# Kernel optimization log

Measured on AMD Instinct MI355X. Metric: run time of the kernel, lower is better.

Reference implementation:

```python
import jax, jax.numpy as jnp
import numpy as np
from jax import lax

B, T, A, L, H, FD = 32, 64, 6, 32, 128, 256


def setup_inputs() -> dict:
    key = jax.random.key(0)
    ks = jax.random.split(key, 24)
    rn = lambda k, s, sc: jax.random.normal(k, s, jnp.float32) * sc
    return {
        "states": rn(ks[0], (B, T, 3, 64, 64), 1.0),
        "actions": rn(ks[1], (B, T, A), 1.0),
        # CNN encoder params (scale ~ 1/sqrt(fan_in))
        "c1_w": rn(ks[2], (32, 3, 4, 4), 0.14), "c1_b": rn(ks[3], (32,), 0.01),
        "c2_w": rn(ks[4], (64, 32, 4, 4), 0.044), "c2_b": rn(ks[5], (64,), 0.01),
        "c3_w": rn(ks[6], (128, 64, 4, 4), 0.031), "c3_b": rn(ks[7], (128,), 0.01),
        "c4_w": rn(ks[8], (256, 128, 4, 4), 0.022), "c4_b": rn(ks[9], (256,), 0.01),
        "fc_w": rn(ks[10], (FD, 256 * 4 * 4), 0.0156), "fc_b": rn(ks[11], (FD,), 0.01),
        # GRUCell params (torch layout: W_ih (3H, in), W_hh (3H, H))
        "gru_wih": rn(ks[12], (3 * H, L + A), 0.16), "gru_whh": rn(ks[13], (3 * H, H), 0.088),
        "gru_bih": rn(ks[14], (3 * H,), 0.01), "gru_bhh": rn(ks[15], (3 * H,), 0.01),
        "prior_w": rn(ks[16], (2 * L, H), 0.088), "prior_b": rn(ks[17], (2 * L,), 0.01),
        "post_w": rn(ks[18], (2 * L, H + FD), 0.05), "post_b": rn(ks[19], (2 * L,), 0.01),
        # reparameterization noise (randn_like in torch), one per (b, t)
        "eps": rn(ks[20], (B, T, L), 1.0),
    }


def _conv(x, w, b):
    # Conv2d(k=4, stride=2, pad=1), NCHW/OIHW
    y = lax.conv_general_dilated(x, w, window_strides=(2, 2),
                                 padding=[(1, 1), (1, 1)],
                                 dimension_numbers=("NCHW", "OIHW", "NCHW"))
    return jax.nn.relu(y + b[None, :, None, None])


def _encode(x, c1_w, c1_b, c2_w, c2_b, c3_w, c3_b, c4_w, c4_b, fc_w, fc_b):
    # x: (N, 3, 64, 64) -> (N, FD)
    x = _conv(x, c1_w, c1_b)
    x = _conv(x, c2_w, c2_b)
    x = _conv(x, c3_w, c3_b)
    x = _conv(x, c4_w, c4_b)  # (N, 256, 4, 4)
    x = x.reshape(x.shape[0], -1)
    return x @ fc_w.T + fc_b


def _gru_cell(x, h, wih, whh, bih, bhh):
    gi = x @ wih.T + bih
    gh = h @ whh.T + bhh
    i_r, i_z, i_n = jnp.split(gi, 3, axis=-1)
    h_r, h_z, h_n = jnp.split(gh, 3, axis=-1)
    r = jax.nn.sigmoid(i_r + h_r)
    z = jax.nn.sigmoid(i_z + h_z)
    n = jnp.tanh(i_n + r * h_n)
    return (1.0 - z) * n + z * h


def reference(states, actions, c1_w, c1_b, c2_w, c2_b, c3_w, c3_b, c4_w, c4_b,
              fc_w, fc_b, gru_wih, gru_whh, gru_bih, gru_bhh,
              prior_w, prior_b, post_w, post_b, eps):
    b, t = states.shape[0], states.shape[1]
    # encoder has no recurrent dependency: encode all frames at once
    feats = _encode(states.reshape(b * t, *states.shape[2:]),
                    c1_w, c1_b, c2_w, c2_b, c3_w, c3_b, c4_w, c4_b,
                    fc_w, fc_b).reshape(b, t, -1)  # (B, T, FD)

    def step(carry, inp):
        h, z = carry
        a_t, f_t, e_t = inp
        h = _gru_cell(jnp.concatenate([z, a_t], -1), h,
                      gru_wih, gru_whh, gru_bih, gru_bhh)
        mu_p, lv_p = jnp.split(h @ prior_w.T + prior_b, 2, axis=-1)
        mu_q, lv_q = jnp.split(jnp.concatenate([h, f_t], -1) @ post_w.T + post_b, 2, axis=-1)
        z = mu_q + jnp.exp(0.5 * lv_q) * e_t
        return (h, z), (mu_p, lv_p, mu_q, lv_q, h, z)

    h0 = jnp.zeros((b, gru_whh.shape[1]), states.dtype)
    z0 = jnp.zeros((b, prior_w.shape[0] // 2), states.dtype)
    xs = (jnp.swapaxes(actions, 0, 1), jnp.swapaxes(feats, 0, 1),
          jnp.swapaxes(eps, 0, 1))
    _, ys = lax.scan(step, (h0, z0), xs)
    # (T, B, d) -> (B, T, d)
    return tuple(jnp.swapaxes(y, 0, 1) for y in ys)
```

## Files before the change

### kernel.cpp

```cpp
#include <hip/hip_runtime.h>
#include <math.h>

#define Bn 32
#define Tn 64
#define An 6
#define Ln 32
#define Hn 128
#define FDn 256
#define Nimg (Bn*Tn)

typedef __attribute__((ext_vector_type(8))) short frag_ab;
typedef __attribute__((ext_vector_type(4))) float frag_cd;
typedef _Float16 h2_t __attribute__((ext_vector_type(2)));

__device__ __forceinline__ float sigmoid_fast(float x){
  return __builtin_amdgcn_rcpf(1.f + __expf(-x));
}
__device__ __forceinline__ float tanh_fast(float x){
  float x2 = fminf(fmaxf(2.f*x, -30.f), 30.f);
  float e = __expf(x2);
  return (e - 1.f) * __builtin_amdgcn_rcpf(e + 1.f);
}

__device__ __forceinline__ unsigned short f2bf(float f){
  unsigned int u = __float_as_uint(f);
  unsigned int r = (u + 0x7fffu + ((u >> 16) & 1u)) >> 16;
  return (unsigned short)r;
}
__device__ __forceinline__ unsigned packh(float a, float b){
  union { h2_t h; unsigned u; } x;
  x.h = (h2_t){(_Float16)a, (_Float16)b};
  return x.u;
}
__device__ __forceinline__ float fdot2u(unsigned a, unsigned b, float c){
  union { unsigned u; h2_t h; } ua, ub;
  ua.u = a; ub.u = b;
#if __has_builtin(__builtin_amdgcn_fdot2)
  return __builtin_amdgcn_fdot2(ua.h, ub.h, c, false);
#else
  return c + (float)ua.h.x*(float)ub.h.x + (float)ua.h.y*(float)ub.h.y;
#endif
}
#define BAR_LDS() asm volatile("s_waitcnt lgkmcnt(0)\n\ts_barrier" ::: "memory")

__device__ __forceinline__ int swz_w(int r, int p){
  return ((r >> 4) << 9) + (p << 7) + ((((r & 15) ^ (p << 2))) << 3);
}
__device__ __forceinline__ int swz_r(int f, int l){
  return (f << 9) + ((l >> 4) << 7) + ((((l & 15) ^ ((l >> 4) << 2))) << 3);
}

__global__ void __launch_bounds__(256)
states_nhwc_kernel(const float* __restrict__ src, unsigned short* __restrict__ dst)
{
  int idx = blockIdx.x*256 + threadIdx.x;
  int n = idx >> 12, pix = idx & 4095;
  const float* s = src + (size_t)n*3*4096 + pix;
  union { unsigned short e[4]; uint2 v; } u;
  u.e[0] = f2bf(s[0]); u.e[1] = f2bf(s[4096]); u.e[2] = f2bf(s[8192]); u.e[3] = 0;
  *(uint2*)(dst + (size_t)idx*4) = u.v;
}

__global__ void __launch_bounds__(256)
prep2_kernel(const float* __restrict__ c1w, const float* __restrict__ c2w,
             const float* __restrict__ c3w, const float* __restrict__ c4w,
             const float* __restrict__ fcw,
             const float* __restrict__ gwhh, const float* __restrict__ gwih,
             const float* __restrict__ prw,  const float* __restrict__ pow_,
             unsigned short* __restrict__ w1p, unsigned short* __restrict__ w2p,
             unsigned short* __restrict__ w3p, unsigned short* __restrict__ w4p,
             unsigned short* __restrict__ wfcp,
             unsigned* __restrict__ g_whh2, unsigned* __restrict__ g_wihz,
             unsigned* __restrict__ g_pr2,  unsigned* __restrict__ g_po2)
{
  const int bid = blockIdx.x, tid = threadIdx.x;
  if (bid < 128){
    int idx = bid*256+tid;
    int k = idx >> 9, r = idx & 511, tap = r >> 5, c = r & 31;
    w2p[idx] = f2bf(c2w[k*512 + c*16 + tap]);
  } else if (bid < 640){
    int idx = (bid-128)*256+tid;
    int k = idx >> 10, r = idx & 1023, tap = r >> 6, c = r & 63;
    w3p[idx] = f2bf(c3w[k*1024 + c*16 + tap]);
  } else if (bid < 2688){
    int idx = (bid-640)*256+tid;
    int k = idx >> 11, r = idx & 2047, tap = r >> 7, c = r & 127;
    w4p[idx] = f2bf(c4w[k*2048 + c*16 + tap]);
  } else if (bid < 6784){
    int idx = (bid-2688)*256+tid;
    int o = idx >> 12, r = idx & 4095, sp = r >> 8, c = r & 255;
    wfcp[idx] = f2bf(fcw[o*4096 + c*16 + sp]);
  } else if (bid < 6792){
    int idx = (bid-6784)*256+tid;
    int k = idx >> 6, r = idx & 63, tap = r >> 2, c = r & 3;
    w1p[idx] = (c < 3) ? f2bf(c1w[k*48 + c*16 + tap]) : (unsigned short)0;
  } else if (bid < 6888){
    int idx = (bid-6792)*256+tid;
    int c = idx / 384, i = idx - c*384;
    g_whh2[idx] = packh(gwhh[i*128 + 2*c], gwhh[i*128 + 2*c + 1]);
  } else if (bid < 6912){
    int idx = (bid-6888)*256+tid;
    int c = idx / 384, i = idx - c*384;
    g_wihz[idx] = packh(gwih[i*38 + 2*c], gwih[i*38 + 2*c + 1]);
  } else if (bid < 6928){
    int idx = (bid-6912)*256+tid;
    int c = idx >> 6, o = idx & 63;
    g_pr2[idx] = packh(prw[o*128 + 2*c], prw[o*128 + 2*c + 1]);
  } else {
    int idx = (bid-6928)*256+tid;
    int c = idx >> 6, o = idx & 63;
    g_po2[idx] = packh(pow_[o*384 + 2*c], pow_[o*384 + 2*c + 1]);
  }
}

__global__ void __launch_bounds__(384)
gia_kernel(const float* __restrict__ actions, const float* __restrict__ gwih,
           const float* __restrict__ bih, float* __restrict__ GIA)
{
  const int tid = threadIdx.x;
  const int bt0 = blockIdx.x * 8;
  __shared__ float ash[48];
  if (tid < 48) ash[tid] = actions[(size_t)bt0*6 + tid];
  float w6[6];
#pragma unroll
  for (int k = 0; k < 6; k++) w6[k] = gwih[tid*38 + 32 + k];
  const float bv = bih[tid];
  __syncthreads();
#pragma unroll
  for (int r = 0; r < 8; r++){
    float v = bv;
#pragma unroll
    for (int k = 0; k < 6; k++) v = fmaf(ash[r*6+k], w6[k], v);
    GIA[(size_t)(bt0 + r)*384 + tid] = v;
  }
}

__global__ void __launch_bounds__(256)
pof_kernel(const float* __restrict__ feats, const float* __restrict__ po_w,
           const float* __restrict__ po_b, float* __restrict__ POF)
{
  const int tid = threadIdx.x;
  const int bt0 = blockIdx.x * 8;
  __shared__ __align__(16) float fsh[8*256];
  const float4* fsrc = (const float4*)(feats + (size_t)bt0*256);
  ((float4*)fsh)[tid]       = fsrc[tid];
  ((float4*)fsh)[tid + 256] = fsrc[tid + 256];
  __syncthreads();
  const float4* w4 = (const float4*)po_w;
  const float4* f4 = (const float4*)fsh;
#pragma unroll
  for (int i = 0; i < 2; i++){
    int item = tid + i*256;
    int row = item >> 6, o = item & 63;
    float4 acc = {0.f,0.f,0.f,0.f};
#pragma unroll 8
    for (int k = 0; k < 64; k++){
      float4 wv = w4[o*96 + 32 + k];
      float4 fv = f4[row*64 + k];
      acc.x = fmaf(wv.x, fv.x, acc.x);
      acc.y = fmaf(wv.y, fv.y, acc.y);
      acc.z = fmaf(wv.z, fv.z, acc.z);
      acc.w = fmaf(wv.w, fv.w, acc.w);
    }
    POF[(size_t)(bt0 + row)*64 + o] = (acc.x + acc.y) + (acc.z + acc.w) + po_b[o];
  }
}

template<int Cin, int IN, int Kout, int OUT, int BN, int LOG_SPB>
__global__ void __launch_bounds__(256)
convN_mfma(const unsigned short* __restrict__ in,
           const unsigned short* __restrict__ wB,
           const float* __restrict__ bias,
           unsigned short* __restrict__ out)
{
  constexpr int SPB = OUT*OUT;
  constexpr int KD  = 16*Cin;
  constexpr int NCH = KD/32;
  constexpr int NFN = BN/32;
  constexpr int BFR = BN/16;
  constexpr int BSL = (BN*4 + 255)/256;
  __shared__ __align__(16) unsigned short Alds[2][8*512];
  __shared__ __align__(16) unsigned short Blds[2][BFR*512];

  const int tid = threadIdx.x;
  const int wave = tid >> 6, lane = tid & 63;
  const unsigned m0 = blockIdx.x * 128;
  const int n0 = blockIdx.y * BN;

  const int p = tid & 3;
  const unsigned short* baseA[2]; int oyA[2], oxA[2]; int AdstI[2];
#pragma unroll
  for (int h = 0; h < 2; h++){
    int r = (tid >> 2) + h*64;
    unsigned m = m0 + r;
    int nimg = m >> LOG_SPB;
    int sp = m & (SPB - 1);
    oyA[h] = sp / OUT; oxA[h] = sp & (OUT - 1);
    baseA[h] = in + (size_t)nimg * IN * IN * Cin;
    AdstI[h] = swz_w(r, p);
  }

  const unsigned short* BsrcH[BSL]; int BdstIH[BSL]; bool bActH[BSL];
#pragma unroll
  for (int h = 0; h < BSL; h++){
    int bn = (tid >> 2) + h*64, pb = tid & 3;
    bActH[h] = bn < BN;
    BsrcH[h] = wB + (size_t)(n0 + bn)*KD + pb*8;
    BdstIH[h] = swz_w(bn, pb);
  }

  const int mhalf = wave >> 1, nhalf = wave & 1;
  frag_cd acc[4][NFN];
#pragma unroll
  for (int i = 0; i < 4; i++)
#pragma unroll
    for (int j = 0; j < NFN; j++) acc[i][j] = (frag_cd){0.f,0.f,0.f,0.f};

  auto loadA = [&](int kt, int h) -> uint4 {
    if constexpr (Cin >= 32){
      constexpr int CPT = Cin/32;
      int tap = kt / CPT;
      int c0 = (kt - tap*CPT)*32;
      int kh = tap >> 2, kw = tap & 3;
      int iy = 2*oyA[h] - 1 + kh;
      int ix = 2*oxA[h] - 1 + kw;
      uint4 v = {0u,0u,0u,0u};
      if ((unsigned)iy < (unsigned)IN && (unsigned)ix < (unsigned)IN)
        v = *(const uint4*)(baseA[h] + ((iy*IN + ix)*Cin + c0 + p*8));
      return v;
    } else {
      int kh = kt*2 + (p >> 1);
      int kw0 = (p & 1)*2;
      int iy = 2*oyA[h] - 1 + kh;
      int ix0 = 2*oxA[h] - 1 + kw0;
      union { uint2 u2[2]; uint4 u4; } v; v.u4 = (uint4){0u,0u,0u,0u};
      bool iyok = (unsigned)iy < (unsigned)IN;
      const unsigned short* rowp = baseA[h] + iy*IN*4;
#pragma unroll
      for (int d = 0; d < 2; d++){
        int ix = ix0 + d;
        if (iyok && (unsigned)ix < (unsigned)IN) v.u2[d] = *(const uint2*)(rowp + ix*4);
      }
      return v.u4;
    }
  };

  const int rdoff = swz_r(0, lane);

  uint4 aR0 = loadA(0,0), aR1 = loadA(0,1);
  uint4 bR[BSL];
#pragma unroll
  for (int h = 0; h < BSL; h++)
    bR[h] = bActH[h] ? *(const uint4*)BsrcH[h] : (uint4){0u,0u,0u,0u};
  *(uint4*)&Alds[0][AdstI[0]] = aR0;
  *(uint4*)&Alds[0][AdstI[1]] = aR1;
#pragma unroll
  for (int h = 0; h < BSL; h++)
    if (bActH[h]) *(uint4*)&Blds[0][BdstIH[h]] = bR[h];
  if (NCH > 1){
    aR0 = loadA(1,0); aR1 = loadA(1,1);
#pragma unroll
    for (int h = 0; h < BSL; h++)
      if (bActH[h]) bR[h] = *(const uint4*)(BsrcH[h] + 32);
  }
  BAR_LDS();

#pragma unroll 2
  for (int kt = 0; kt < NCH; kt++){
    const int cur = kt & 1, nxt = cur ^ 1;
    if (kt + 1 < NCH){
      *(uint4*)&Alds[nxt][AdstI[0]] = aR0;
      *(uint4*)&Alds[nxt][AdstI[1]] = aR1;
#pragma unroll
      for (int h = 0; h < BSL; h++)
        if (bActH[h]) *(uint4*)&Blds[nxt][BdstIH[h]] = bR[h];
      if (kt + 2 < NCH){
        aR0 = loadA(kt+2, 0);
        aR1 = loadA(kt+2, 1);
#pragma unroll
        for (int h = 0; h < BSL; h++)
          if (bActH[h]) bR[h] = *(const uint4*)(BsrcH[h] + (kt+2)*32);
      }
    }
    frag_ab a[4], bf[NFN];
#pragma unroll
    for (int i = 0; i < 4; i++)
      a[i] = *(const frag_ab*)&Alds[cur][(((mhalf<<2) + i) << 9) + rdoff];
#pragma unroll
    for (int j = 0; j < NFN; j++)
      bf[j] = *(const frag_ab*)&Blds[cur][((nhalf*NFN + j) << 9) + rdoff];
#pragma unroll
    for (int i = 0; i < 4; i++)
#pragma unroll
      for (int j = 0; j < NFN; j++)
        acc[i][j] = __builtin_amdgcn_mfma_f32_16x16x32_bf16(a[i], bf[j], acc[i][j], 0, 0, 0);
    BAR_LDS();
  }

  const unsigned mb = m0 + mhalf*64 + ((lane >> 4) << 2);
#pragma unroll
  for (int j = 0; j < NFN; j++){
    const int kg = n0 + nhalf*(NFN*16) + j*16 + (lane & 15);
    const float bv = bias[kg];
#pragma unroll
    for (int i = 0; i < 4; i++){
#pragma unroll
      for (int r = 0; r < 4; r++){
        unsigned mg = mb + i*16 + r;
        out[(size_t)mg*Kout + kg] = f2bf(fmaxf(acc[i][j][r] + bv, 0.f));
      }
    }
  }
}

__global__ void __launch_bounds__(256)
fc_mfma2(const unsigned short* __restrict__ A, const unsigned short* __restrict__ wB,
         const float* __restrict__ bias, float* __restrict__ outF)
{
  constexpr int KD = 4096, NCH = KD/32;
  __shared__ __align__(16) unsigned short Alds[2][4*512];
  __shared__ __align__(16) unsigned short Blds[2][4*512];

  const int tid = threadIdx.x, wave = tid >> 6, lane = tid & 63;
  const int m0 = blockIdx.x * 64, n0 = blockIdx.y * 64;
  const int r = tid >> 2, pc = tid & 3;
  const unsigned short* Asrc = A + (size_t)(m0 + r)*KD + pc*8;
  const unsigned short* Bsrc = wB + (size_t)(n0 + r)*KD + pc*8;
  const int wI = swz_w(r, pc);
  const int mh = wave >> 1, nh = wave & 1;
  const int rdoff = swz_r(0, lane);

  frag_cd acc[2][2];
#pragma unroll
  for (int i = 0; i < 2; i++)
#pragma unroll
    for (int j = 0; j < 2; j++) acc[i][j] = (frag_cd){0.f,0.f,0.f,0.f};

  uint4 aP = *(const uint4*)Asrc, bP = *(const uint4*)Bsrc;
  *(uint4*)&Alds[0][wI] = aP;
  *(uint4*)&Blds[0][wI] = bP;
  aP = *(const uint4*)(Asrc + 32);
  bP = *(const uint4*)(Bsrc + 32);
  BAR_LDS();

#pragma unroll 2
  for (int kt = 0; kt < NCH; kt++){
    const int cur = kt & 1, nxt = cur ^ 1;
    if (kt + 1 < NCH){
      *(uint4*)&Alds[nxt][wI] = aP;
      *(uint4*)&Blds[nxt][wI] = bP;
      if (kt + 2 < NCH){
        aP = *(const uint4*)(Asrc + (kt+2)*32);
        bP = *(const uint4*)(Bsrc + (kt+2)*32);
      }
    }
    frag_ab a[2], b[2];
#pragma unroll
    for (int i = 0; i < 2; i++) a[i] = *(const frag_ab*)&Alds[cur][(((mh<<1)+i) << 9) + rdoff];
#pragma unroll
    for (int j = 0; j < 2; j++) b[j] = *(const frag_ab*)&Blds[cur][(((nh<<1)+j) << 9) + rdoff];
#pragma unroll
    for (int i = 0; i < 2; i++)
#pragma unroll
      for (int j = 0; j < 2; j++)
        acc[i][j] = __builtin_amdgcn_mfma_f32_16x16x32_bf16(a[i], b[j], acc[i][j], 0, 0, 0);
    BAR_LDS();
  }

  const int mb = m0 + mh*32 + ((lane >> 4) << 2);
#pragma unroll
  for (int j = 0; j < 2; j++){
    const int kg = n0 + nh*32 + j*16 + (lane & 15);
    const float bv = bias[kg];
#pragma unroll
    for (int i = 0; i < 2; i++)
#pragma unroll
      for (int rr = 0; rr < 4; rr++)
        outF[(size_t)(mb + i*16 + rr)*256 + kg] = acc[i][j][rr] + bv;
  }
}

__global__ void __launch_bounds__(384)
rssm_scan5(const unsigned* __restrict__ g_whh2, const unsigned* __restrict__ g_wihz,
           const unsigned* __restrict__ g_pr2,  const unsigned* __restrict__ g_po2,
           const float* __restrict__ GIA, const float* __restrict__ POF,
           const float* __restrict__ eps, const float* __restrict__ bhh,
           const float* __restrict__ pr_b, float* __restrict__ out)
{
  __shared__ __align__(16) _Float16 sh_h[128];
  __shared__ __align__(16) _Float16 sh_z[32];
  __shared__ float sh_gi[384];
  __shared__ float sh_gh[384];

  const int b = blockIdx.x, tid = threadIdx.x;
  const int wv = tid >> 6, lane = tid & 63;

  unsigned whh2[64];
#pragma unroll
  for (int c = 0; c < 64; c++) whh2[c] = g_whh2[c*384 + tid];
  unsigned wihz[16];
#pragma unroll
  for (int c = 0; c < 16; c++) wihz[c] = g_wihz[c*384 + tid];
  const float bhh_i = bhh[tid];

  unsigned wpx[64];
  float prbr = 0.f;
  if (wv == 0){
#pragma unroll
    for (int c = 0; c < 64; c++) wpx[c] = g_pr2[c*64 + lane];
    prbr = pr_b[lane];
  } else if (wv == 1){
#pragma unroll
    for (int c = 0; c < 64; c++) wpx[c] = g_po2[c*64 + lane];
  }

  unsigned hsu[64];
#pragma unroll
  for (int c = 0; c < 64; c++) hsu[c] = 0u;

  if (tid < 128) sh_h[tid] = (_Float16)0.f;
  if (tid < 32)  sh_z[tid] = (_Float16)0.f;

  float GIAr = GIA[(size_t)(b*64)*384 + tid];
  float POFr = (wv == 1) ? POF[(size_t)(b*64)*64 + lane] : 0.f;
  float epsr = (wv == 1 && lane < 32) ? eps[(size_t)(b*64)*32 + lane] : 0.f;

  const int OFF_MUP = 0;
  const int OFF_LVP = Bn*Tn*Ln;
  const int OFF_MUQ = 2*Bn*Tn*Ln;
  const int OFF_LVQ = 3*Bn*Tn*Ln;
  const int OFF_H   = 4*Bn*Tn*Ln;
  const int OFF_Z   = 4*Bn*Tn*Ln + Bn*Tn*Hn;

  float hreg = 0.f;
  __syncthreads();

  for (int t = 0; t < Tn; t++){
    const size_t bt = (size_t)b*64 + t;

    {
      const uint4* Z4 = (const uint4*)sh_z;
      uint4 z0 = Z4[0], z1 = Z4[1], z2 = Z4[2], z3 = Z4[3];
      float a0 = GIAr, a1 = 0.f, a2 = 0.f, a3 = 0.f;
      a0 = fdot2u(wihz[0],  z0.x, a0); a1 = fdot2u(wihz[1],  z0.y, a1);
      a2 = fdot2u(wihz[2],  z0.z, a2); a3 = fdot2u(wihz[3],  z0.w, a3);
      a0 = fdot2u(wihz[4],  z1.x, a0); a1 = fdot2u(wihz[5],  z1.y, a1);
      a2 = fdot2u(wihz[6],  z1.z, a2); a3 = fdot2u(wihz[7],  z1.w, a3);
      a0 = fdot2u(wihz[8],  z2.x, a0); a1 = fdot2u(wihz[9],  z2.y, a1);
      a2 = fdot2u(wihz[10], z2.z, a2); a3 = fdot2u(wihz[11], z2.w, a3);
      a0 = fdot2u(wihz[12], z3.x, a0); a1 = fdot2u(wihz[13], z3.y, a1);
      a2 = fdot2u(wihz[14], z3.z, a2); a3 = fdot2u(wihz[15], z3.w, a3);

      float g0 = bhh_i, g1 = 0.f, g2 = 0.f, g3 = 0.f;
#pragma unroll
      for (int c = 0; c < 64; c += 4){
        g0 = fdot2u(whh2[c],   hsu[c],   g0);
        g1 = fdot2u(whh2[c+1], hsu[c+1], g1);
        g2 = fdot2u(whh2[c+2], hsu[c+2], g2);
        g3 = fdot2u(whh2[c+3], hsu[c+3], g3);
      }
      sh_gi[tid] = (a0 + a1) + (a2 + a3);
      sh_gh[tid] = (g0 + g1) + (g2 + g3);
    }
    if (t < Tn-1) GIAr = GIA[(bt+1)*384 + tid];
    BAR_LDS();

    if (tid < 128){
      const float r  = sigmoid_fast(sh_gi[tid]       + sh_gh[tid]);
      const float zg = sigmoid_fast(sh_gi[128 + tid] + sh_gh[128 + tid]);
      const float nn = tanh_fast(fmaf(r, sh_gh[256 + tid], sh_gi[256 + tid]));
      hreg = (1.f - zg)*nn + zg*hreg;
      sh_h[tid] = (_Float16)hreg;
      out[OFF_H + bt*128 + tid] = hreg;
    }
    BAR_LDS();

    {
      unsigned hv = ((const unsigned*)sh_h)[lane];
#pragma unroll
      for (int c = 0; c < 64; c++) hsu[c] = __builtin_amdgcn_readlane(hv, c);
    }
    if (wv == 0){
      float p0 = prbr, p1 = 0.f, p2 = 0.f, p3 = 0.f;
#pragma unroll
      for (int c = 0; c < 64; c += 4){
        p0 = fdot2u(wpx[c],   hsu[c],   p0);
        p1 = fdot2u(wpx[c+1], hsu[c+1], p1);
        p2 = fdot2u(wpx[c+2], hsu[c+2], p2);
        p3 = fdot2u(wpx[c+3], hsu[c+3], p3);
      }
      const float p = (p0 + p1) + (p2 + p3);
      if (lane < 32) out[OFF_MUP + bt*32 + lane] = p;
      else           out[OFF_LVP + bt*32 + (lane - 32)] = p;
    } else if (wv == 1){
      float p0 = POFr, p1 = 0.f, p2 = 0.f, p3 = 0.f;
#pragma unroll
      for (int c = 0; c < 64; c += 4){
        p0 = fdot2u(wpx[c],   hsu[c],   p0);
        p1 = fdot2u(wpx[c+1], hsu[c+1], p1);
        p2 = fdot2u(wpx[c+2], hsu[c+2], p2);
        p3 = fdot2u(wpx[c+3], hsu[c+3], p3);
      }
      const float p = (p0 + p1) + (p2 + p3);
      const float q = __shfl_xor(p, 32);
      if (lane < 32){
        out[OFF_MUQ + bt*32 + lane] = p;
        const float zz = fmaf(__expf(0.5f*q), epsr, p);
        sh_z[lane] = (_Float16)zz;
        out[OFF_Z + bt*32 + lane] = zz;
      } else {
        out[OFF_LVQ + bt*32 + (lane - 32)] = p;
      }
      if (t < Tn-1){
        POFr = POF[(bt+1)*64 + lane];
        if (lane < 32) epsr = eps[(bt+1)*32 + lane];
      }
    }
    BAR_LDS();
  }
}

extern "C" void kernel_launch(void* const* d_in, const int* in_sizes, int n_in,
                              void* d_out, int out_size, void* d_ws, size_t ws_size,
                              hipStream_t stream)
{
  const float* states = (const float*)d_in[0];
  const float* actions= (const float*)d_in[1];
  const float* c1_w = (const float*)d_in[2];  const float* c1_b = (const float*)d_in[3];
  const float* c2_w = (const float*)d_in[4];  const float* c2_b = (const float*)d_in[5];
  const float* c3_w = (const float*)d_in[6];  const float* c3_b = (const float*)d_in[7];
  const float* c4_w = (const float*)d_in[8];  const float* c4_b = (const float*)d_in[9];
  const float* fc_w = (const float*)d_in[10]; const float* fc_b = (const float*)d_in[11];
  const float* gwih = (const float*)d_in[12]; const float* gwhh = (const float*)d_in[13];
  const float* gbih = (const float*)d_in[14]; const float* gbhh = (const float*)d_in[15];
  const float* pr_w = (const float*)d_in[16]; const float* pr_b = (const float*)d_in[17];
  const float* po_w = (const float*)d_in[18]; const float* po_b = (const float*)d_in[19];
  const float* eps  = (const float*)d_in[20];

  char* p = (char*)d_ws;
  auto alloc = [&](size_t bytes){ char* r = p; p += (bytes + 255) & ~255ULL; return r; };

  unsigned short* statesB = (unsigned short*)alloc((size_t)Nimg*4096*4*2);
  unsigned short* act1    = (unsigned short*)alloc((size_t)Nimg*1024*32*2);
  unsigned short* act2    = (unsigned short*)alloc((size_t)Nimg*256*64*2);
  unsigned short* act3    = (unsigned short*)alloc((size_t)Nimg*64*128*2);
  unsigned short* act4    = (unsigned short*)alloc((size_t)Nimg*16*256*2);
  float*          feats   = (float*)alloc((size_t)Nimg*FDn*4);
  unsigned short* w1p     = (unsigned short*)alloc(32*64*2);
  unsigned short* w2p     = (unsigned short*)alloc((size_t)64*512*2);
  unsigned short* w3p     = (unsigned short*)alloc((size_t)128*1024*2);
  unsigned short* w4p     = (unsigned short*)alloc((size_t)256*2048*2);
  unsigned short* wfcp    = (unsigned short*)alloc((size_t)256*4096*2);
  unsigned* g_whh2 = (unsigned*)alloc((size_t)24576*4);
  unsigned* g_wihz = (unsigned*)alloc((size_t)6144*4);
  unsigned* g_pr2  = (unsigned*)alloc((size_t)4096*4);
  unsigned* g_po2  = (unsigned*)alloc((size_t)4096*4);
  float*    GIAb   = (float*)alloc((size_t)786432*4);
  float*    POFb   = (float*)alloc((size_t)Nimg*64*4);

  states_nhwc_kernel<<<Nimg*4096/256, 256, 0, stream>>>(states, statesB);
  prep2_kernel<<<6944, 256, 0, stream>>>(c1_w, c2_w, c3_w, c4_w, fc_w,
                                         gwhh, gwih, pr_w, po_w,
                                         w1p, w2p, w3p, w4p, wfcp,
                                         g_whh2, g_wihz, g_pr2, g_po2);
  gia_kernel<<<Nimg/8, 384, 0, stream>>>(actions, gwih, gbih, GIAb);

  convN_mfma<4,64,32,32,32,10>  <<< dim3(Nimg*1024/128, 1), 256, 0, stream >>>(statesB, w1p, c1_b, act1);
  convN_mfma<32,32,64,16,64,8>  <<< dim3(Nimg*256/128, 1), 256, 0, stream >>>(act1, w2p, c2_b, act2);
  convN_mfma<64,16,128,8,128,6> <<< dim3(Nimg*64/128, 1), 256, 0, stream >>>(act2, w3p, c3_b, act3);
  convN_mfma<128,8,256,4,128,4> <<< dim3(Nimg*16/128, 2), 256, 0, stream >>>(act3, w4p, c4_b, act4);

  fc_mfma2<<< dim3(Nimg/64, 4), 256, 0, stream >>>(act4, wfcp, fc_b, feats);
  pof_kernel<<< Nimg/8, 256, 0, stream >>>(feats, po_w, po_b, POFb);

  rssm_scan5<<< Bn, 384, 0, stream >>>(g_whh2, g_wihz, g_pr2, g_po2,
                                       GIAb, POFb, eps, gbhh, pr_b, (float*)d_out);
}
```

Baseline: 572.7 us.

## Split recurrent scan K dimension across two thread halves with 768-thread blocks

The per-batch RSSM scan kernel doubles its block to 768 threads so each gate row's hidden and latent dot products are split in two along K. Partial sums land in separate shared arrays and are combined in the gate step. The prior and posterior projections are also split over two waves, with a shuffle reduction across the lane halves. The aim is to shorten the serial per-timestep dependency chain and cut register pressure per thread. The cost is extra shared-memory traffic and reductions, and possible occupancy or scheduling limits from the 768-thread block.

```diff
diff --git a/kernel.cpp b/kernel.cpp
--- a/kernel.cpp
+++ b/kernel.cpp
@@ -380,8 +380,8 @@
   }
 }
 
-__global__ void __launch_bounds__(384)
-rssm_scan5(const unsigned* __restrict__ g_whh2, const unsigned* __restrict__ g_wihz,
+__global__ __attribute__((amdgpu_waves_per_eu(3, 3))) void __launch_bounds__(768)
+rssm_scan6(const unsigned* __restrict__ g_whh2, const unsigned* __restrict__ g_wihz,
            const unsigned* __restrict__ g_pr2,  const unsigned* __restrict__ g_po2,
            const float* __restrict__ GIA, const float* __restrict__ POF,
            const float* __restrict__ eps, const float* __restrict__ bhh,
@@ -390,40 +390,52 @@
   __shared__ __align__(16) _Float16 sh_h[128];
   __shared__ __align__(16) _Float16 sh_z[32];
   __shared__ float sh_gi[384];
-  __shared__ float sh_gh[384];
+  __shared__ float sh_zi1[384];
+  __shared__ float sh_gh0[384];
+  __shared__ float sh_gh1[384];
 
   const int b = blockIdx.x, tid = threadIdx.x;
   const int wv = tid >> 6, lane = tid & 63;
-
-  unsigned whh2[64];
-#pragma unroll
-  for (int c = 0; c < 64; c++) whh2[c] = g_whh2[c*384 + tid];
-  unsigned wihz[16];
-#pragma unroll
-  for (int c = 0; c < 16; c++) wihz[c] = g_wihz[c*384 + tid];
-  const float bhh_i = bhh[tid];
-
-  unsigned wpx[64];
-  float prbr = 0.f;
-  if (wv == 0){
-#pragma unroll
-    for (int c = 0; c < 64; c++) wpx[c] = g_pr2[c*64 + lane];
-    prbr = pr_b[lane];
-  } else if (wv == 1){
-#pragma unroll
-    for (int c = 0; c < 64; c++) wpx[c] = g_po2[c*64 + lane];
-  }
-
-  unsigned hsu[64];
-#pragma unroll
-  for (int c = 0; c < 64; c++) hsu[c] = 0u;
-
-  if (tid < 128) sh_h[tid] = (_Float16)0.f;
-  if (tid < 32)  sh_z[tid] = (_Float16)0.f;
-
-  float GIAr = GIA[(size_t)(b*64)*384 + tid];
-  float POFr = (wv == 1) ? POF[(size_t)(b*64)*64 + lane] : 0.f;
-  float epsr = (wv == 1 && lane < 32) ? eps[(size_t)(b*64)*32 + lane] : 0.f;
+  const int kh = (wv >= 6) ? 1 : 0;
+  const int nn = tid - (kh ? 384 : 0);
+
+  unsigned whhH[32];
+#pragma unroll
+  for (int j = 0; j < 32; j++) whhH[j] = g_whh2[(kh*32 + j)*384 + nn];
+  unsigned wihzH[8];
+#pragma unroll
+  for (int j = 0; j < 8; j++) wihzH[j] = g_wihz[(kh*8 + j)*384 + nn];
+  const float bhh_i = kh ? 0.f : bhh[nn];
+
+  const bool isPR = (wv == 0) || (wv == 6);
+  const bool isPO = (wv == 1) || (wv == 7);
+  const int khl = lane >> 5;
+  int o = 0;
+  if (isPR)      o = ((wv == 6) ? 32 : 0) + (lane & 31);
+  else if (isPO) o = ((wv == 7) ? 16 : 0) + ((lane & 16) << 1) + (lane & 15);
+  unsigned wpx[32];
+#pragma unroll
+  for (int j = 0; j < 32; j++) wpx[j] = 0u;
+  if (isPR){
+#pragma unroll
+    for (int j = 0; j < 32; j++) wpx[j] = g_pr2[(khl*32 + j)*64 + o];
+  } else if (isPO){
+#pragma unroll
+    for (int j = 0; j < 32; j++) wpx[j] = g_po2[(khl*32 + j)*64 + o];
+  }
+  const float prbr = isPR ? pr_b[o] : 0.f;
+
+  unsigned hsu[32];
+#pragma unroll
+  for (int j = 0; j < 32; j++) hsu[j] = 0u;
+
+  if (tid < 64) ((unsigned*)sh_h)[tid] = 0u;
+  if (tid < 16) ((unsigned*)sh_z)[tid] = 0u;
+
+  const bool muLane = isPO && (lane < 16);
+  float GIAr = (kh == 0) ? GIA[(size_t)(b*64)*384 + nn] : 0.f;
+  float POFr = (isPO && lane < 32) ? POF[(size_t)(b*64)*64 + o] : 0.f;
+  float epsr = muLane ? eps[(size_t)(b*64)*32 + o] : 0.f;
 
   const int OFF_MUP = 0;
   const int OFF_LVP = Bn*Tn*Ln;
@@ -440,36 +452,37 @@
 
     {
       const uint4* Z4 = (const uint4*)sh_z;
-      uint4 z0 = Z4[0], z1 = Z4[1], z2 = Z4[2], z3 = Z4[3];
-      float a0 = GIAr, a1 = 0.f, a2 = 0.f, a3 = 0.f;
-      a0 = fdot2u(wihz[0],  z0.x, a0); a1 = fdot2u(wihz[1],  z0.y, a1);
-      a2 = fdot2u(wihz[2],  z0.z, a2); a3 = fdot2u(wihz[3],  z0.w, a3);
-      a0 = fdot2u(wihz[4],  z1.x, a0); a1 = fdot2u(wihz[5],  z1.y, a1);
-      a2 = fdot2u(wihz[6],  z1.z, a2); a3 = fdot2u(wihz[7],  z1.w, a3);
-      a0 = fdot2u(wihz[8],  z2.x, a0); a1 = fdot2u(wihz[9],  z2.y, a1);
-      a2 = fdot2u(wihz[10], z2.z, a2); a3 = fdot2u(wihz[11], z2.w, a3);
-      a0 = fdot2u(wihz[12], z3.x, a0); a1 = fdot2u(wihz[13], z3.y, a1);
-      a2 = fdot2u(wihz[14], z3.z, a2); a3 = fdot2u(wihz[15], z3.w, a3);
+      uint4 zlo = Z4[kh*2], zhi = Z4[kh*2 + 1];
+      float a0 = (kh == 0) ? GIAr : 0.f, a1 = 0.f;
+      a0 = fdot2u(wihzH[0], zlo.x, a0); a1 = fdot2u(wihzH[1], zlo.y, a1);
+      a0 = fdot2u(wihzH[2], zlo.z, a0); a1 = fdot2u(wihzH[3], zlo.w, a1);
+      a0 = fdot2u(wihzH[4], zhi.x, a0); a1 = fdot2u(wihzH[5], zhi.y, a1);
+      a0 = fdot2u(wihzH[6], zhi.z, a0); a1 = fdot2u(wihzH[7], zhi.w, a1);
 
       float g0 = bhh_i, g1 = 0.f, g2 = 0.f, g3 = 0.f;
 #pragma unroll
-      for (int c = 0; c < 64; c += 4){
-        g0 = fdot2u(whh2[c],   hsu[c],   g0);
-        g1 = fdot2u(whh2[c+1], hsu[c+1], g1);
-        g2 = fdot2u(whh2[c+2], hsu[c+2], g2);
-        g3 = fdot2u(whh2[c+3], hsu[c+3], g3);
-      }
-      sh_gi[tid] = (a0 + a1) + (a2 + a3);
-      sh_gh[tid] = (g0 + g1) + (g2 + g3);
-    }
-    if (t < Tn-1) GIAr = GIA[(bt+1)*384 + tid];
+      for (int j = 0; j < 32; j += 4){
+        g0 = fdot2u(whhH[j],   hsu[j],   g0);
+        g1 = fdot2u(whhH[j+1], hsu[j+1], g1);
+        g2 = fdot2u(whhH[j+2], hsu[j+2], g2);
+        g3 = fdot2u(whhH[j+3], hsu[j+3], g3);
+      }
+      const float gpart = (g0 + g1) + (g2 + g3);
+      if (kh == 0){ sh_gi[nn]  = a0 + a1; sh_gh0[nn] = gpart; }
+      else        { sh_zi1[nn] = a0 + a1; sh_gh1[nn] = gpart; }
+    }
+    if (t < Tn-1 && kh == 0) GIAr = GIA[(bt+1)*384 + nn];
     BAR_LDS();
 
     if (tid < 128){
-      const float r  = sigmoid_fast(sh_gi[tid]       + sh_gh[tid]);
-      const float zg = sigmoid_fast(sh_gi[128 + tid] + sh_gh[128 + tid]);
-      const float nn = tanh_fast(fmaf(r, sh_gh[256 + tid], sh_gi[256 + tid]));
-      hreg = (1.f - zg)*nn + zg*hreg;
+      const float gr = (sh_gi[tid]     + sh_zi1[tid])     + (sh_gh0[tid]     + sh_gh1[tid]);
+      const float gz = (sh_gi[128+tid] + sh_zi1[128+tid]) + (sh_gh0[128+tid] + sh_gh1[128+tid]);
+      const float in_ = sh_gi[256+tid] + sh_zi1[256+tid];
+      const float hn_ = sh_gh0[256+tid] + sh_gh1[256+tid];
+      const float r  = sigmoid_fast(gr);
+      const float zg = sigmoid_fast(gz);
+      const float nngate = tanh_fast(fmaf(r, hn_, in_));
+      hreg = (1.f - zg)*nngate + zg*hreg;
       sh_h[tid] = (_Float16)hreg;
       out[OFF_H + bt*128 + tid] = hreg;
     }
@@ -478,42 +491,44 @@
     {
       unsigned hv = ((const unsigned*)sh_h)[lane];
 #pragma unroll
-      for (int c = 0; c < 64; c++) hsu[c] = __builtin_amdgcn_readlane(hv, c);
-    }
-    if (wv == 0){
-      float p0 = prbr, p1 = 0.f, p2 = 0.f, p3 = 0.f;
-#pragma unroll
-      for (int c = 0; c < 64; c += 4){
-        p0 = fdot2u(wpx[c],   hsu[c],   p0);
-        p1 = fdot2u(wpx[c+1], hsu[c+1], p1);
-        p2 = fdot2u(wpx[c+2], hsu[c+2], p2);
-        p3 = fdot2u(wpx[c+3], hsu[c+3], p3);
-      }
-      const float p = (p0 + p1) + (p2 + p3);
-      if (lane < 32) out[OFF_MUP + bt*32 + lane] = p;
-      else           out[OFF_LVP + bt*32 + (lane - 32)] = p;
-    } else if (wv == 1){
-      float p0 = POFr, p1 = 0.f, p2 = 0.f, p3 = 0.f;
-#pragma unroll
-      for (int c = 0; c < 64; c += 4){
-        p0 = fdot2u(wpx[c],   hsu[c],   p0);
-        p1 = fdot2u(wpx[c+1], hsu[c+1], p1);
-        p2 = fdot2u(wpx[c+2], hsu[c+2], p2);
-        p3 = fdot2u(wpx[c+3], hsu[c+3], p3);
-      }
-      const float p = (p0 + p1) + (p2 + p3);
-      const float q = __shfl_xor(p, 32);
-      if (lane < 32){
-        out[OFF_MUQ + bt*32 + lane] = p;
-        const float zz = fmaf(__expf(0.5f*q), epsr, p);
-        sh_z[lane] = (_Float16)zz;
-        out[OFF_Z + bt*32 + lane] = zz;
+      for (int j = 0; j < 32; j++) hsu[j] = __builtin_amdgcn_readlane(hv, kh*32 + j);
+    }
+    if (isPR || isPO){
+      float p0 = 0.f, p1 = 0.f, p2 = 0.f, p3 = 0.f;
+      const uint4* H4 = (const uint4*)sh_h;
+#pragma unroll
+      for (int j4 = 0; j4 < 8; j4++){
+        uint4 hb = H4[khl*8 + j4];
+        p0 = fdot2u(wpx[4*j4+0], hb.x, p0);
+        p1 = fdot2u(wpx[4*j4+1], hb.y, p1);
+        p2 = fdot2u(wpx[4*j4+2], hb.z, p2);
+        p3 = fdot2u(wpx[4*j4+3], hb.w, p3);
+      }
+      float part = (p0 + p1) + (p2 + p3);
+      float pfull = part + __shfl_xor(part, 32);
+      if (isPR){
+        if (lane < 32){
+          const float p = pfull + prbr;
+          if (wv == 0) out[OFF_MUP + bt*32 + o] = p;
+          else         out[OFF_LVP + bt*32 + (o - 32)] = p;
+        }
       } else {
-        out[OFF_LVQ + bt*32 + (lane - 32)] = p;
-      }
-      if (t < Tn-1){
-        POFr = POF[(bt+1)*64 + lane];
-        if (lane < 32) epsr = eps[(bt+1)*32 + lane];
+        if (lane < 32){
+          const float p = pfull + POFr;
+          const float q = __shfl_xor(p, 16);
+          if (lane < 16){
+            out[OFF_MUQ + bt*32 + o] = p;
+            const float zz = fmaf(__expf(0.5f*q), epsr, p);
+            sh_z[o] = (_Float16)zz;
+            out[OFF_Z + bt*32 + o] = zz;
+          } else {
+            out[OFF_LVQ + bt*32 + (o - 32)] = p;
+          }
+        }
+        if (t < Tn-1){
+          if (lane < 32) POFr = POF[(bt+1)*64 + o];
+          if (muLane)    epsr = eps[(bt+1)*32 + o];
+        }
       }
     }
     BAR_LDS();
@@ -573,6 +588,6 @@
   fc_mfma2<<< dim3(Nimg/64, 4), 256, 0, stream >>>(act4, wfcp, fc_b, feats);
   pof_kernel<<< Nimg/8, 256, 0, stream >>>(feats, po_w, po_b, POFb);
 
-  rssm_scan5<<< Bn, 384, 0, stream >>>(g_whh2, g_wihz, g_pr2, g_po2,
+  rssm_scan6<<< Bn, 768, 0, stream >>>(g_whh2, g_wihz, g_pr2, g_po2,
                                        GIAb, POFb, eps, gbhh, pr_b, (float*)d_out);
 }
```

Measured after the change: 595.0 us. 1.04x slower.
